# Kernel optimization log

Measured on AMD Instinct MI355X. Metric: run time of the kernel, lower is better.

## Reference

```python
import jax, jax.numpy as jnp
import numpy as np

B, F, G, K = 8192, 8192, 2048, 8


def setup_inputs() -> dict:
    key = jax.random.key(0)
    k1, k2, k3 = jax.random.split(key, 3)
    x = jax.random.normal(k1, (B, F), dtype=jnp.float32)
    group_idx = jax.random.randint(k2, (G, K), 0, F, dtype=jnp.int64)
    # HeNormal-ish init over fan_in=K for each (K,1) group weight
    w = jax.random.normal(k3, (G, K), dtype=jnp.float32) * jnp.sqrt(2.0 / K)
    return {"x": x, "group_idx": group_idx, "w": w}


def reference(x, group_idx, w):
    # Fused equivalent of: for each group g, gather x[:, idx_g] then matmul
    # with w_g (K,1), stack over groups, squeeze -> [B, G].
    gathered = x[:, group_idx]              # [B, G, K] single gather
    return jnp.einsum('bgk,gk->bg', gathered, w)  # [B, G]
```

## Files before the change

### kernel.cpp

```cpp
#include <hip/hip_runtime.h>


#define GC_B 8192
#define GC_F 8192
#define GC_G 2048
#define GC_K 8
#define GC_THREADS 256

__global__ __launch_bounds__(GC_THREADS) void gc_kernel(
    const float* __restrict__ x,
    const int* __restrict__ gidx,
    const float* __restrict__ w,
    float* __restrict__ out)
{
    __shared__ float xrow[GC_F];

    const int b = blockIdx.x;
    const float4* __restrict__ xr4 =
        (const float4*)(x + (size_t)b * GC_F);

    float4* xrow4 = (float4*)xrow;
    #pragma unroll
    for (int i = 0; i < GC_F / 4 / GC_THREADS; ++i) {
        const int p = threadIdx.x + i * GC_THREADS;
        xrow4[p] = xr4[p];
    }
    __syncthreads();

    float* orow = out + (size_t)b * GC_G;
    #pragma unroll
    for (int j = 0; j < GC_G / GC_THREADS; ++j) {
        const int g = threadIdx.x + j * GC_THREADS;
        const int4* ip = (const int4*)(gidx + g * GC_K);
        const float4* wp = (const float4*)(w + g * GC_K);
        const int4 i0 = ip[0];
        const int4 i1 = ip[1];
        const float4 w0 = wp[0];
        const float4 w1 = wp[1];
        float s = xrow[i0.x] * w0.x;
        s += xrow[i0.y] * w0.y;
        s += xrow[i0.z] * w0.z;
        s += xrow[i0.w] * w0.w;
        s += xrow[i1.x] * w1.x;
        s += xrow[i1.y] * w1.y;
        s += xrow[i1.z] * w1.z;
        s += xrow[i1.w] * w1.w;
        orow[g] = s;
    }
}

extern "C" void kernel_launch(void* const* d_in, const int* in_sizes, int n_in,
                              void* d_out, int out_size, void* d_ws, size_t ws_size,
                              hipStream_t stream) {
    const float* x = (const float*)d_in[0];
    const int* gidx = (const int*)d_in[1];
    const float* w = (const float*)d_in[2];
    float* out = (float*)d_out;

    gc_kernel<<<GC_B, GC_THREADS, 0, stream>>>(x, gidx, w, out);
}
```

Before: 383.9 us.

## Process two batch rows per block with interleaved float2 shared layout

Each block now handles two rows of x, storing them interleaved as float2 in shared memory so that each gathered index yields both rows' values with one LDS. The index and weight loads are reused across the two rows, halving their global/cache traffic per output. Block size grows to 512 threads with a 64KB shared footprint, which may limit occupancy to fewer blocks per CU.

```diff
diff --git a/kernel.cpp b/kernel.cpp
--- a/kernel.cpp
+++ b/kernel.cpp
@@ -5,47 +5,61 @@
 #define GC_F 8192
 #define GC_G 2048
 #define GC_K 8
-#define GC_THREADS 256
+#define GC_T 512
+#define GC_RPB 2
 
-__global__ __launch_bounds__(GC_THREADS) void gc_kernel(
+__global__ __launch_bounds__(GC_T, 4) void gc_kernel(
     const float* __restrict__ x,
     const int* __restrict__ gidx,
     const float* __restrict__ w,
     float* __restrict__ out)
 {
-    __shared__ float xrow[GC_F];
+    __shared__ __align__(16) float2 xld[GC_F];
 
-    const int b = blockIdx.x;
-    const float4* __restrict__ xr4 =
-        (const float4*)(x + (size_t)b * GC_F);
+    const int b0 = blockIdx.x * GC_RPB;
+    const float2* __restrict__ r0 = (const float2*)(x + (size_t)b0 * GC_F);
+    const float2* __restrict__ r1 = (const float2*)(x + ((size_t)b0 + 1) * GC_F);
 
-    float4* xrow4 = (float4*)xrow;
     #pragma unroll
-    for (int i = 0; i < GC_F / 4 / GC_THREADS; ++i) {
-        const int p = threadIdx.x + i * GC_THREADS;
-        xrow4[p] = xr4[p];
+    for (int i = 0; i < GC_F / 2 / GC_T; ++i) {
+        const int c = threadIdx.x + i * GC_T;
+        const float2 a = r0[c];
+        const float2 b = r1[c];
+        float4 v;
+        v.x = a.x; v.y = b.x; v.z = a.y; v.w = b.y;
+        *(float4*)(&xld[2 * c]) = v;
     }
     __syncthreads();
 
-    float* orow = out + (size_t)b * GC_G;
-    #pragma unroll
-    for (int j = 0; j < GC_G / GC_THREADS; ++j) {
-        const int g = threadIdx.x + j * GC_THREADS;
+    float* o0 = out + (size_t)b0 * GC_G;
+    float* o1 = out + ((size_t)b0 + 1) * GC_G;
+
+    #pragma unroll 2
+    for (int j = 0; j < GC_G / GC_T; ++j) {
+        const int g = threadIdx.x + j * GC_T;
         const int4* ip = (const int4*)(gidx + g * GC_K);
         const float4* wp = (const float4*)(w + g * GC_K);
         const int4 i0 = ip[0];
         const int4 i1 = ip[1];
         const float4 w0 = wp[0];
         const float4 w1 = wp[1];
-        float s = xrow[i0.x] * w0.x;
-        s += xrow[i0.y] * w0.y;
-        s += xrow[i0.z] * w0.z;
-        s += xrow[i0.w] * w0.w;
-        s += xrow[i1.x] * w1.x;
-        s += xrow[i1.y] * w1.y;
-        s += xrow[i1.z] * w1.z;
-        s += xrow[i1.w] * w1.w;
-        orow[g] = s;
+
+        float2 v0 = xld[i0.x];
+        float2 v1 = xld[i0.y];
+        float2 v2 = xld[i0.z];
+        float2 v3 = xld[i0.w];
+        float2 v4 = xld[i1.x];
+        float2 v5 = xld[i1.y];
+        float2 v6 = xld[i1.z];
+        float2 v7 = xld[i1.w];
+
+        float s0 = v0.x * w0.x + v1.x * w0.y + v2.x * w0.z + v3.x * w0.w
+                 + v4.x * w1.x + v5.x * w1.y + v6.x * w1.z + v7.x * w1.w;
+        float s1 = v0.y * w0.x + v1.y * w0.y + v2.y * w0.z + v3.y * w0.w
+                 + v4.y * w1.x + v5.y * w1.y + v6.y * w1.z + v7.y * w1.w;
+
+        o0[g] = s0;
+        o1[g] = s1;
     }
 }
 
@@ -57,5 +71,5 @@
     const float* w = (const float*)d_in[2];
     float* out = (float*)d_out;
 
-    gc_kernel<<<GC_B, GC_THREADS, 0, stream>>>(x, gidx, w, out);
+    gc_kernel<<<GC_B / GC_RPB, GC_T, 0, stream>>>(x, gidx, w, out);
 }
```

Measured after the change: 370.4 us. -3.5%, faster.
